# Optimization experiments

Hardware: AMD Instinct MI355X
Metric: run time of the kernel (lower is better)

Reference implementation:

```python
import jax, jax.numpy as jnp
import numpy as np

B, N = 64, 128          # batch, nodes
D = 3                   # feature_dim
E = 1                   # edge_dim
M = 16                  # m_dim (lucidrains EGNN default)
L = 2                   # number_of_layers
EIN = 2 * D + 1 + E     # edge MLP input dim = 8


def setup_inputs() -> dict:
    key = jax.random.key(0)
    ks = jax.random.split(key, 24)
    s = 0.1

    def w(k, shape):
        return jax.random.normal(k, shape, dtype=jnp.float32) * s

    return {
        "t": jax.random.uniform(ks[0], (B, N, 1), dtype=jnp.float32),
        "coors": jax.random.normal(ks[1], (B, N, 2), dtype=jnp.float32),
        "vel": jax.random.normal(ks[2], (B, N, 2), dtype=jnp.float32),
        # per-layer EGNN params, stacked over L layers
        "We1": w(ks[3], (L, EIN, 2 * EIN)), "be1": jnp.zeros((L, 2 * EIN), jnp.float32),
        "We2": w(ks[4], (L, 2 * EIN, M)),   "be2": jnp.zeros((L, M), jnp.float32),
        "Wc1": w(ks[5], (L, M, 4 * M)),     "bc1": jnp.zeros((L, 4 * M), jnp.float32),
        "Wc2": w(ks[6], (L, 4 * M, 1)),     "bc2": jnp.zeros((L, 1), jnp.float32),
        "Wv": w(ks[7], (L, D, 1)),          "bv": jnp.ones((L, 1), jnp.float32),
        # 1x1 conv head (kernel size 1 -> plain channel matmul)
        "Wconv1": w(ks[8], (32, 4)), "bconv1": jnp.zeros((32,), jnp.float32),
        "Wconv2": w(ks[9], (4, 32)), "bconv2": jnp.zeros((4,), jnp.float32),
    }


def _egnn_forward(t, coors, vel, We1, be1, We2, be2, Wc1, bc1, Wc2, bc2, Wv, bv,
                  Wconv1, bconv1, Wconv2, bconv2):
    silu = jax.nn.silu
    selu = jax.nn.selu
    b, n, _ = coors.shape
    feats = jnp.broadcast_to(t, (b, n, D))          # t.repeat(1,1,feature_dim)
    edges = jnp.ones((b, n, n, E), dtype=coors.dtype)
    hi = jnp.broadcast_to(feats[:, :, None, :], (b, n, n, D))
    hj = jnp.broadcast_to(feats[:, None, :, :], (b, n, n, D))

    for l in range(L):
        rel = coors[:, :, None, :] - coors[:, None, :, :]      # b i j 2
        dist = jnp.sum(rel * rel, axis=-1, keepdims=True)      # b i j 1
        e_in = jnp.concatenate([hi, hj, dist, edges], axis=-1) # b i j 8
        # edge MLP: Linear -> SiLU -> Linear -> SiLU
        m = silu(e_in @ We1[l] + be1[l])
        m = silu(m @ We2[l] + be2[l])                          # b i j M
        # coors MLP: SiLU -> Linear -> SiLU -> Linear -> scalar weight per edge
        h = silu(silu(m) @ Wc1[l] + bc1[l])
        w_ij = (h @ Wc2[l] + bc2[l])[..., 0]                   # b i j
        agg = jnp.einsum('bij,bijc->bic', w_ij, rel)           # b i 2
        # velocity update: phi_v(h_i) * v_i + aggregated relative-coor messages
        phi_v = feats @ Wv[l] + bv[l]                          # b n 1
        vel = phi_v * vel + agg
        coors = coors + vel
        # EGNN_layer wrapper applies SELU to coors and vel
        coors = selu(coors)
        vel = selu(vel)

    # conv head: concat channels (coors 2 + vel 2 = 4), two 1x1 convs
    x = selu(jnp.concatenate([coors, vel], axis=-1))           # b n 4
    x = selu(jnp.einsum('bnc,oc->bno', x, Wconv1) + bconv1)    # b n 32
    y = jnp.einsum('bnc,oc->bno', x, Wconv2) + bconv2          # b n 4
    return y[..., 0:2], y[..., 2:4]


def reference(t, coors, vel, We1, be1, We2, be2, Wc1, bc1, Wc2, bc2, Wv, bv,
              Wconv1, bconv1, Wconv2, bconv2):
    return _egnn_forward(t, coors, vel, We1, be1, We2, be2, Wc1, bc1, Wc2, bc2,
                         Wv, bv, Wconv1, bconv1, Wconv2, bconv2)
```

## Files before the change

### kernel.cpp

```cpp
#include <hip/hip_runtime.h>


#define NB 64
#define NN 128

typedef __attribute__((ext_vector_type(8))) short short8;
typedef __attribute__((ext_vector_type(4))) float floatx4;

__device__ __forceinline__ unsigned short f2bf(float x) {
    unsigned u = __float_as_uint(x);
    return (unsigned short)((u + 0x7FFFu + ((u >> 16) & 1u)) >> 16);
}
__device__ __forceinline__ float bf2f(unsigned short b) {
    return __uint_as_float(((unsigned)b) << 16);
}
__device__ __forceinline__ unsigned packbf(float x, float y) {
    unsigned xb = __float_as_uint(x) + 0x8000u;
    unsigned yb = __float_as_uint(y) + 0x8000u;
    return __builtin_amdgcn_perm(yb, xb, 0x07060302u);
}
__device__ __forceinline__ float silu_f(float x) {
    float e = __expf(-x);
    return x * __builtin_amdgcn_rcpf(1.0f + e);
}
__device__ __forceinline__ float selu_f(float x) {
    const float alpha = 1.6732632423543772f;
    const float scale = 1.0507009873554805f;
    float neg = alpha * (__expf(x) - 1.0f);
    return scale * (x > 0.0f ? x : neg);
}

__global__ __launch_bounds__(128) void egnn_prep(
    const float* __restrict__ We1, const float* __restrict__ be1,
    const float* __restrict__ We2, const float* __restrict__ Wc1,
    float* __restrict__ prep)
{
    const int layer = threadIdx.x >> 6;
    const int l = threadIdx.x & 63;
    const int q = l >> 4, em = l & 15;
    const float* We1l = We1 + layer * 128;
    const float* be1l = be1 + layer * 16;
    const float* We2l = We2 + layer * 256;
    const float* Wc1l = Wc1 + layer * 1024;
    float* P = prep + layer * 2048;

    if (l < 16) {
        P[l]      = We1l[l] + We1l[16 + l] + We1l[32 + l];
        P[16 + l] = We1l[48 + l] + We1l[64 + l] + We1l[80 + l];
        P[32 + l] = We1l[96 + l];
        P[48 + l] = We1l[112 + l] + be1l[l];
    }
    {
        unsigned wb[4];
#pragma unroll
        for (int d = 0; d < 4; ++d) {
            unsigned short sv[2];
#pragma unroll
            for (int e = 0; e < 2; ++e) {
                int k = q * 8 + 2 * d + e;
                float w = We2l[(k & 15) * 16 + em];
                unsigned short hv = f2bf(w);
                unsigned short lv = f2bf(w - bf2f(hv));
                sv[e] = (k < 16) ? hv : lv;
            }
            wb[d] = (unsigned)sv[0] | ((unsigned)sv[1] << 16);
        }
        *(uint4*)((unsigned*)(P + 64) + l * 4) = make_uint4(wb[0], wb[1], wb[2], wb[3]);
    }
#pragma unroll
    for (int f = 0; f < 4; ++f) {
        unsigned wc[4];
#pragma unroll
        for (int d = 0; d < 4; ++d) {
            unsigned short sv[2];
#pragma unroll
            for (int e = 0; e < 2; ++e) {
                int k = q * 8 + 2 * d + e;
                float w = Wc1l[(k & 15) * 64 + 16 * f + em];
                unsigned short hv = f2bf(w);
                unsigned short lv = f2bf(w - bf2f(hv));
                sv[e] = (k < 16) ? hv : lv;
            }
            wc[d] = (unsigned)sv[0] | ((unsigned)sv[1] << 16);
        }
        *(uint4*)((unsigned*)(P + 320) + l * 16 + f * 4) = make_uint4(wc[0], wc[1], wc[2], wc[3]);
    }
}

template <bool DO_HEAD>
__global__ __launch_bounds__(256) void egnn_layer(
    const float* __restrict__ t,
    const float* __restrict__ coors_in,
    const float* __restrict__ vel_in,
    const float* __restrict__ prep,
    const float* __restrict__ be2,
    const float* __restrict__ bc1,
    const float* __restrict__ Wc2, const float* __restrict__ bc2,
    const float* __restrict__ Wv,  const float* __restrict__ bv,
    const float* __restrict__ Wconv1, const float* __restrict__ bconv1,
    const float* __restrict__ Wconv2, const float* __restrict__ bconv2,
    int layer,
    float* __restrict__ coors_out, float* __restrict__ vel_out,
    float* __restrict__ out)
{
    const int l   = threadIdx.x & 63;
    const int wvi = threadIdx.x >> 6;
    const int row = blockIdx.x * 4 + wvi;
    const int b   = row >> 7;
    const int i   = row & 127;
    const int q   = l >> 4;
    const int em  = l & 15;

    const float* P    = prep + layer * 2048;
    const float* be2l = be2 + layer * 16;
    const float* bc1l = bc1 + layer * 64;
    const float* Wc2l = Wc2 + layer * 64;
    const float  wv_s = Wv[layer * 3 + 0] + Wv[layer * 3 + 1] + Wv[layer * 3 + 2];
    const float  bvl  = bv[layer];

    const float4 a4 = *(const float4*)(P + 0  + q * 4);
    const float4 b4 = *(const float4*)(P + 16 + q * 4);
    const float4 c4 = *(const float4*)(P + 32 + q * 4);
    const float4 d4 = *(const float4*)(P + 48 + q * 4);
    const short8 wB = __builtin_bit_cast(short8, *(const uint4*)((const unsigned*)(P + 64) + l * 4));
    short8 wC[4];
#pragma unroll
    for (int f = 0; f < 4; ++f)
        wC[f] = __builtin_bit_cast(short8, *(const uint4*)((const unsigned*)(P + 320) + l * 16 + f * 4));
    const floatx4 biasB = __builtin_bit_cast(floatx4, *(const float4*)(be2l + q * 4));
    floatx4 biasC[4];
    float4 w2[4];
#pragma unroll
    for (int f = 0; f < 4; ++f) {
        biasC[f] = __builtin_bit_cast(floatx4, *(const float4*)(bc1l + f * 16 + q * 4));
        w2[f]    = *(const float4*)(Wc2l + f * 16 + q * 4);
    }
    const float bc2q = (q == 0) ? bc2[layer] : 0.0f;

    const float ti = t[b * NN + i];
    const float2* cin = (const float2*)coors_in + b * NN;
    const float2 ci = cin[i];

    const int sA = em + ((q & 1) << 5);
    const int sB = sA + 16;

    float ax = 0.0f, ay = 0.0f;

#pragma unroll 2
    for (int tt = 0; tt < 8; ++tt) {
        const int j = tt * 16 + em;
        const float tj = t[b * NN + j];
        const float2 cj = cin[j];
        const float rx = ci.x - cj.x, ry = ci.y - cj.y;
        const float dist = rx * rx + ry * ry;

        float sA0 = fmaf(ti, a4.x, fmaf(tj, b4.x, fmaf(dist, c4.x, d4.x)));
        float sA1 = fmaf(ti, a4.y, fmaf(tj, b4.y, fmaf(dist, c4.y, d4.y)));
        float sA2 = fmaf(ti, a4.z, fmaf(tj, b4.z, fmaf(dist, c4.z, d4.z)));
        float sA3 = fmaf(ti, a4.w, fmaf(tj, b4.w, fmaf(dist, c4.w, d4.w)));
        unsigned P0 = packbf(silu_f(sA0), silu_f(sA1));
        unsigned P1 = packbf(silu_f(sA2), silu_f(sA3));
        uint4 tb;
        tb.x = (unsigned)__shfl((int)P0, sA, 64);
        tb.y = (unsigned)__shfl((int)P1, sA, 64);
        tb.z = (unsigned)__shfl((int)P0, sB, 64);
        tb.w = (unsigned)__shfl((int)P1, sB, 64);
        short8 bB = __builtin_bit_cast(short8, tb);

        floatx4 accB = __builtin_amdgcn_mfma_f32_16x16x32_bf16(wB, bB, biasB, 0, 0, 0);
        unsigned Q0 = packbf(silu_f(silu_f(accB[0])), silu_f(silu_f(accB[1])));
        unsigned Q1 = packbf(silu_f(silu_f(accB[2])), silu_f(silu_f(accB[3])));
        uint4 tc;
        tc.x = (unsigned)__shfl((int)Q0, sA, 64);
        tc.y = (unsigned)__shfl((int)Q1, sA, 64);
        tc.z = (unsigned)__shfl((int)Q0, sB, 64);
        tc.w = (unsigned)__shfl((int)Q1, sB, 64);
        short8 bC = __builtin_bit_cast(short8, tc);

        floatx4 h0 = __builtin_amdgcn_mfma_f32_16x16x32_bf16(wC[0], bC, biasC[0], 0, 0, 0);
        floatx4 h1 = __builtin_amdgcn_mfma_f32_16x16x32_bf16(wC[1], bC, biasC[1], 0, 0, 0);
        floatx4 h2 = __builtin_amdgcn_mfma_f32_16x16x32_bf16(wC[2], bC, biasC[2], 0, 0, 0);
        floatx4 h3 = __builtin_amdgcn_mfma_f32_16x16x32_bf16(wC[3], bC, biasC[3], 0, 0, 0);

        float wp = bc2q;
#pragma unroll
        for (int r = 0; r < 4; ++r) wp = fmaf(silu_f(h0[r]), w2[0].x * 0.0f + ((const float*)&w2[0])[r], wp);
#pragma unroll
        for (int r = 0; r < 4; ++r) wp = fmaf(silu_f(h1[r]), ((const float*)&w2[1])[r], wp);
#pragma unroll
        for (int r = 0; r < 4; ++r) wp = fmaf(silu_f(h2[r]), ((const float*)&w2[2])[r], wp);
#pragma unroll
        for (int r = 0; r < 4; ++r) wp = fmaf(silu_f(h3[r]), ((const float*)&w2[3])[r], wp);

        ax = fmaf(wp, rx, ax);
        ay = fmaf(wp, ry, ay);
    }

#pragma unroll
    for (int m = 32; m >= 1; m >>= 1) {
        ax += __shfl_xor(ax, m, 64);
        ay += __shfl_xor(ay, m, 64);
    }

    const float2 vi = ((const float2*)vel_in + b * NN)[i];
    const float phi = ti * wv_s + bvl;
    float vx = fmaf(phi, vi.x, ax);
    float vy = fmaf(phi, vi.y, ay);
    float cx = selu_f(ci.x + vx);
    float cy = selu_f(ci.y + vy);
    vx = selu_f(vx); vy = selu_f(vy);

    if (!DO_HEAD) {
        if (l == 0) {
            ((float2*)coors_out + b * NN)[i] = make_float2(cx, cy);
            ((float2*)vel_out + b * NN)[i]   = make_float2(vx, vy);
        }
    } else {
        const float x0 = selu_f(cx), x1 = selu_f(cy);
        const float x2 = selu_f(vx), x3 = selu_f(vy);
        const int c = l & 31;
        const float4 w1 = *(const float4*)(Wconv1 + c * 4);
        const float xc = selu_f(bconv1[c] + fmaf(x0, w1.x, fmaf(x1, w1.y, fmaf(x2, w1.z, x3 * w1.w))));
        float y0 = xc * Wconv2[c];
        float y1 = xc * Wconv2[32 + c];
        float y2 = xc * Wconv2[64 + c];
        float y3 = xc * Wconv2[96 + c];
#pragma unroll
        for (int m = 16; m >= 1; m >>= 1) {
            y0 += __shfl_xor(y0, m, 64);
            y1 += __shfl_xor(y1, m, 64);
            y2 += __shfl_xor(y2, m, 64);
            y3 += __shfl_xor(y3, m, 64);
        }
        if (l == 0) {
            const int idx = (b * NN + i) * 2;
            *(float2*)(out + idx) = make_float2(y0 + bconv2[0], y1 + bconv2[1]);
            *(float2*)(out + NB * NN * 2 + idx) = make_float2(y2 + bconv2[2], y3 + bconv2[3]);
        }
    }
}

extern "C" void kernel_launch(void* const* d_in, const int* in_sizes, int n_in,
                              void* d_out, int out_size, void* d_ws, size_t ws_size,
                              hipStream_t stream) {
    const float* t      = (const float*)d_in[0];
    const float* coors  = (const float*)d_in[1];
    const float* vel    = (const float*)d_in[2];
    const float* We1    = (const float*)d_in[3];
    const float* be1    = (const float*)d_in[4];
    const float* We2    = (const float*)d_in[5];
    const float* be2    = (const float*)d_in[6];
    const float* Wc1    = (const float*)d_in[7];
    const float* bc1    = (const float*)d_in[8];
    const float* Wc2    = (const float*)d_in[9];
    const float* bc2    = (const float*)d_in[10];
    const float* Wv     = (const float*)d_in[11];
    const float* bv     = (const float*)d_in[12];
    const float* Wconv1 = (const float*)d_in[13];
    const float* bconv1 = (const float*)d_in[14];
    const float* Wconv2 = (const float*)d_in[15];
    const float* bconv2 = (const float*)d_in[16];
    float* out = (float*)d_out;

    float* ws     = (float*)d_ws;
    float* coors1 = ws;
    float* vel1   = ws + NB * NN * 2;
    float* prep   = ws + 2 * NB * NN * 2;

    egnn_prep<<<dim3(1), dim3(128), 0, stream>>>(We1, be1, We2, Wc1, prep);

    const dim3 grid(2048), block(256);

    egnn_layer<false><<<grid, block, 0, stream>>>(
        t, coors, vel, prep, be2, bc1, Wc2, bc2, Wv, bv,
        Wconv1, bconv1, Wconv2, bconv2, 0, coors1, vel1, nullptr);

    egnn_layer<true><<<grid, block, 0, stream>>>(
        t, coors1, vel1, prep, be2, bc1, Wc2, bc2, Wv, bv,
        Wconv1, bconv1, Wconv2, bconv2, 1, nullptr, nullptr, out);
}
```

Before: 152.8 us.

## Fold log2e scaling into precomputed weights and use native exp2 for SiLU

```diff
diff --git a/kernel.cpp b/kernel.cpp
--- a/kernel.cpp
+++ b/kernel.cpp
@@ -3,6 +3,8 @@
 
 #define NB 64
 #define NN 128
+#define LOG2E 1.4426950408889634f
+#define LN2f  0.6931471805599453f
 
 typedef __attribute__((ext_vector_type(8))) short short8;
 typedef __attribute__((ext_vector_type(4))) float floatx4;
@@ -19,9 +21,9 @@
     unsigned yb = __float_as_uint(y) + 0x8000u;
     return __builtin_amdgcn_perm(yb, xb, 0x07060302u);
 }
-__device__ __forceinline__ float silu_f(float x) {
-    float e = __expf(-x);
-    return x * __builtin_amdgcn_rcpf(1.0f + e);
+__device__ __forceinline__ float silu_s(float xs) {
+    float e = __builtin_amdgcn_exp2f(-xs);
+    return xs * __builtin_amdgcn_rcpf(1.0f + e);
 }
 __device__ __forceinline__ float selu_f(float x) {
     const float alpha = 1.6732632423543772f;
@@ -32,7 +34,9 @@
 
 __global__ __launch_bounds__(128) void egnn_prep(
     const float* __restrict__ We1, const float* __restrict__ be1,
-    const float* __restrict__ We2, const float* __restrict__ Wc1,
+    const float* __restrict__ We2, const float* __restrict__ be2,
+    const float* __restrict__ Wc1, const float* __restrict__ bc1,
+    const float* __restrict__ Wc2,
     float* __restrict__ prep)
 {
     const int layer = threadIdx.x >> 6;
@@ -41,15 +45,22 @@
     const float* We1l = We1 + layer * 128;
     const float* be1l = be1 + layer * 16;
     const float* We2l = We2 + layer * 256;
+    const float* be2l = be2 + layer * 16;
     const float* Wc1l = Wc1 + layer * 1024;
+    const float* bc1l = bc1 + layer * 64;
+    const float* Wc2l = Wc2 + layer * 64;
     float* P = prep + layer * 2048;
 
     if (l < 16) {
-        P[l]      = We1l[l] + We1l[16 + l] + We1l[32 + l];
-        P[16 + l] = We1l[48 + l] + We1l[64 + l] + We1l[80 + l];
-        P[32 + l] = We1l[96 + l];
-        P[48 + l] = We1l[112 + l] + be1l[l];
-    }
+        P[l]      = (We1l[l] + We1l[16 + l] + We1l[32 + l]) * LOG2E;
+        P[16 + l] = (We1l[48 + l] + We1l[64 + l] + We1l[80 + l]) * LOG2E;
+        P[32 + l] = We1l[96 + l] * LOG2E;
+        P[48 + l] = (We1l[112 + l] + be1l[l]) * LOG2E;
+        P[1344 + l] = be2l[l] * LOG2E;
+    }
+    P[1360 + l] = bc1l[l] * LOG2E;
+    P[1424 + l] = Wc2l[l] * LN2f;
+
     {
         unsigned wb[4];
 #pragma unroll
@@ -88,14 +99,12 @@
 }
 
 template <bool DO_HEAD>
-__global__ __launch_bounds__(256) void egnn_layer(
+__global__ __launch_bounds__(256, 8) void egnn_layer(
     const float* __restrict__ t,
     const float* __restrict__ coors_in,
     const float* __restrict__ vel_in,
     const float* __restrict__ prep,
-    const float* __restrict__ be2,
-    const float* __restrict__ bc1,
-    const float* __restrict__ Wc2, const float* __restrict__ bc2,
+    const float* __restrict__ bc2,
     const float* __restrict__ Wv,  const float* __restrict__ bv,
     const float* __restrict__ Wconv1, const float* __restrict__ bconv1,
     const float* __restrict__ Wconv2, const float* __restrict__ bconv2,
@@ -111,10 +120,7 @@
     const int q   = l >> 4;
     const int em  = l & 15;
 
-    const float* P    = prep + layer * 2048;
-    const float* be2l = be2 + layer * 16;
-    const float* bc1l = bc1 + layer * 64;
-    const float* Wc2l = Wc2 + layer * 64;
+    const float* P = prep + layer * 2048;
     const float  wv_s = Wv[layer * 3 + 0] + Wv[layer * 3 + 1] + Wv[layer * 3 + 2];
     const float  bvl  = bv[layer];
 
@@ -127,17 +133,18 @@
 #pragma unroll
     for (int f = 0; f < 4; ++f)
         wC[f] = __builtin_bit_cast(short8, *(const uint4*)((const unsigned*)(P + 320) + l * 16 + f * 4));
-    const floatx4 biasB = __builtin_bit_cast(floatx4, *(const float4*)(be2l + q * 4));
+    const floatx4 biasB = __builtin_bit_cast(floatx4, *(const float4*)(P + 1344 + q * 4));
     floatx4 biasC[4];
     float4 w2[4];
 #pragma unroll
     for (int f = 0; f < 4; ++f) {
-        biasC[f] = __builtin_bit_cast(floatx4, *(const float4*)(bc1l + f * 16 + q * 4));
-        w2[f]    = *(const float4*)(Wc2l + f * 16 + q * 4);
+        biasC[f] = __builtin_bit_cast(floatx4, *(const float4*)(P + 1360 + f * 16 + q * 4));
+        w2[f]    = *(const float4*)(P + 1424 + f * 16 + q * 4);
     }
     const float bc2q = (q == 0) ? bc2[layer] : 0.0f;
 
-    const float ti = t[b * NN + i];
+    const float* tptr = t + b * NN;
+    const float ti = tptr[i];
     const float2* cin = (const float2*)coors_in + b * NN;
     const float2 ci = cin[i];
 
@@ -146,36 +153,43 @@
 
     float ax = 0.0f, ay = 0.0f;
 
-#pragma unroll 2
+    float tj_n = tptr[em];
+    float2 cj_n = cin[em];
+
+#pragma unroll 1
     for (int tt = 0; tt < 8; ++tt) {
-        const int j = tt * 16 + em;
-        const float tj = t[b * NN + j];
-        const float2 cj = cin[j];
+        const float tj = tj_n;
+        const float2 cj = cj_n;
+        if (tt < 7) {
+            const int jn = (tt + 1) * 16 + em;
+            tj_n = tptr[jn];
+            cj_n = cin[jn];
+        }
         const float rx = ci.x - cj.x, ry = ci.y - cj.y;
-        const float dist = rx * rx + ry * ry;
-
-        float sA0 = fmaf(ti, a4.x, fmaf(tj, b4.x, fmaf(dist, c4.x, d4.x)));
-        float sA1 = fmaf(ti, a4.y, fmaf(tj, b4.y, fmaf(dist, c4.y, d4.y)));
-        float sA2 = fmaf(ti, a4.z, fmaf(tj, b4.z, fmaf(dist, c4.z, d4.z)));
-        float sA3 = fmaf(ti, a4.w, fmaf(tj, b4.w, fmaf(dist, c4.w, d4.w)));
-        unsigned P0 = packbf(silu_f(sA0), silu_f(sA1));
-        unsigned P1 = packbf(silu_f(sA2), silu_f(sA3));
+        const float dist = fmaf(rx, rx, ry * ry);
+
+        float s0 = fmaf(ti, a4.x, fmaf(tj, b4.x, fmaf(dist, c4.x, d4.x)));
+        float s1 = fmaf(ti, a4.y, fmaf(tj, b4.y, fmaf(dist, c4.y, d4.y)));
+        float s2 = fmaf(ti, a4.z, fmaf(tj, b4.z, fmaf(dist, c4.z, d4.z)));
+        float s3 = fmaf(ti, a4.w, fmaf(tj, b4.w, fmaf(dist, c4.w, d4.w)));
+        unsigned P0 = packbf(silu_s(s0), silu_s(s1));
+        unsigned P1 = packbf(silu_s(s2), silu_s(s3));
         uint4 tb;
         tb.x = (unsigned)__shfl((int)P0, sA, 64);
         tb.y = (unsigned)__shfl((int)P1, sA, 64);
         tb.z = (unsigned)__shfl((int)P0, sB, 64);
         tb.w = (unsigned)__shfl((int)P1, sB, 64);
-        short8 bB = __builtin_bit_cast(short8, tb);
-
-        floatx4 accB = __builtin_amdgcn_mfma_f32_16x16x32_bf16(wB, bB, biasB, 0, 0, 0);
-        unsigned Q0 = packbf(silu_f(silu_f(accB[0])), silu_f(silu_f(accB[1])));
-        unsigned Q1 = packbf(silu_f(silu_f(accB[2])), silu_f(silu_f(accB[3])));
+
+        floatx4 accB = __builtin_amdgcn_mfma_f32_16x16x32_bf16(
+            wB, __builtin_bit_cast(short8, tb), biasB, 0, 0, 0);
+        unsigned Q0 = packbf(silu_s(silu_s(accB[0])), silu_s(silu_s(accB[1])));
+        unsigned Q1 = packbf(silu_s(silu_s(accB[2])), silu_s(silu_s(accB[3])));
         uint4 tc;
         tc.x = (unsigned)__shfl((int)Q0, sA, 64);
         tc.y = (unsigned)__shfl((int)Q1, sA, 64);
         tc.z = (unsigned)__shfl((int)Q0, sB, 64);
         tc.w = (unsigned)__shfl((int)Q1, sB, 64);
-        short8 bC = __builtin_bit_cast(short8, tc);
+        const short8 bC = __builtin_bit_cast(short8, tc);
 
         floatx4 h0 = __builtin_amdgcn_mfma_f32_16x16x32_bf16(wC[0], bC, biasC[0], 0, 0, 0);
         floatx4 h1 = __builtin_amdgcn_mfma_f32_16x16x32_bf16(wC[1], bC, biasC[1], 0, 0, 0);
@@ -184,13 +198,13 @@
 
         float wp = bc2q;
 #pragma unroll
-        for (int r = 0; r < 4; ++r) wp = fmaf(silu_f(h0[r]), w2[0].x * 0.0f + ((const float*)&w2[0])[r], wp);
-#pragma unroll
-        for (int r = 0; r < 4; ++r) wp = fmaf(silu_f(h1[r]), ((const float*)&w2[1])[r], wp);
-#pragma unroll
-        for (int r = 0; r < 4; ++r) wp = fmaf(silu_f(h2[r]), ((const float*)&w2[2])[r], wp);
-#pragma unroll
-        for (int r = 0; r < 4; ++r) wp = fmaf(silu_f(h3[r]), ((const float*)&w2[3])[r], wp);
+        for (int r = 0; r < 4; ++r) wp = fmaf(silu_s(h0[r]), ((const float*)&w2[0])[r], wp);
+#pragma unroll
+        for (int r = 0; r < 4; ++r) wp = fmaf(silu_s(h1[r]), ((const float*)&w2[1])[r], wp);
+#pragma unroll
+        for (int r = 0; r < 4; ++r) wp = fmaf(silu_s(h2[r]), ((const float*)&w2[2])[r], wp);
+#pragma unroll
+        for (int r = 0; r < 4; ++r) wp = fmaf(silu_s(h3[r]), ((const float*)&w2[3])[r], wp);
 
         ax = fmaf(wp, rx, ax);
         ay = fmaf(wp, ry, ay);
@@ -203,7 +217,7 @@
     }
 
     const float2 vi = ((const float2*)vel_in + b * NN)[i];
-    const float phi = ti * wv_s + bvl;
+    const float phi = fmaf(ti, wv_s, bvl);
     float vx = fmaf(phi, vi.x, ax);
     float vy = fmaf(phi, vi.y, ay);
     float cx = selu_f(ci.x + vx);
@@ -267,15 +281,15 @@
     float* vel1   = ws + NB * NN * 2;
     float* prep   = ws + 2 * NB * NN * 2;
 
-    egnn_prep<<<dim3(1), dim3(128), 0, stream>>>(We1, be1, We2, Wc1, prep);
+    egnn_prep<<<dim3(1), dim3(128), 0, stream>>>(We1, be1, We2, be2, Wc1, bc1, Wc2, prep);
 
     const dim3 grid(2048), block(256);
 
     egnn_layer<false><<<grid, block, 0, stream>>>(
-        t, coors, vel, prep, be2, bc1, Wc2, bc2, Wv, bv,
+        t, coors, vel, prep, bc2, Wv, bv,
         Wconv1, bconv1, Wconv2, bconv2, 0, coors1, vel1, nullptr);
 
     egnn_layer<true><<<grid, block, 0, stream>>>(
-        t, coors1, vel1, prep, be2, bc1, Wc2, bc2, Wv, bv,
+        t, coors1, vel1, prep, bc2, Wv, bv,
         Wconv1, bconv1, Wconv2, bconv2, 1, nullptr, nullptr, out);
 }
```

Result: slower. 318.1 us (+108.1%).
